# Optimization experiments

Hardware: AMD Instinct MI355X
Metric: run time of the kernel (lower is better)

The kernel has to match this reference:

```python
import jax, jax.numpy as jnp
import numpy as np

HEADS, DIM, SEQ_LEN, MEM_LEN, CMEM_LEN, CMEM_RATIO = 16, 1024, 512, 512, 128, 4
DIM_H = DIM // HEADS


def shift(x):
    # relative-position shift trick, same as torch version
    *lead, i, j = x.shape
    x = jnp.concatenate([x, jnp.zeros((*lead, i, i), x.dtype)], -1)
    l = i + j - 1
    x = x.reshape(*lead, -1)
    pad = (-x.shape[-1]) % l
    x = jnp.concatenate([x, jnp.zeros((*lead, pad), x.dtype)], -1)
    x = x.reshape(*lead, -1, l)
    return x[..., :i, i - 1:]


def merge_heads(t):
    b, n, _ = t.shape
    return t.reshape(b, n, HEADS, DIM_H).transpose(0, 2, 1, 3)  # [b,h,n,dh]


def conv_compress(mem, conv_w, conv_b):
    # Conv1d(dim, dim, k=ratio, stride=ratio) == blockwise einsum
    b, L, e = mem.shape
    blocks = mem.reshape(b, L // CMEM_RATIO, CMEM_RATIO, e)
    return jnp.einsum('bmri,oir->bmo', blocks, conv_w) + conv_b


def full_attn(q, k, v):
    dots = jnp.einsum('bhid,bhjd->bhij', q, k) * (q.shape[-1] ** -0.5)
    attn = jax.nn.softmax(dots, axis=-1)
    return jnp.einsum('bhij,bhjd->bhid', attn, v)


def setup_inputs() -> dict:
    key = jax.random.key(0)
    ks = jax.random.split(key, 10)
    b = 8
    kv_len = CMEM_LEN + MEM_LEN + SEQ_LEN
    s = 0.02
    return {
        'x': jax.random.normal(ks[0], (b, SEQ_LEN, DIM), jnp.float32),
        'mem': jax.random.normal(ks[1], (b, MEM_LEN, DIM), jnp.float32),
        'cmem': jax.random.normal(ks[2], (b, CMEM_LEN, DIM), jnp.float32),
        'pos_emb': jax.random.normal(ks[3], (HEADS, kv_len, DIM_H), jnp.float32),
        'Wq': jax.random.normal(ks[4], (DIM, DIM), jnp.float32) * s,
        'Wkv': jax.random.normal(ks[5], (DIM, 2 * DIM), jnp.float32) * s,
        'Wout': jax.random.normal(ks[6], (DIM, DIM), jnp.float32) * s,
        'bout': jnp.zeros((DIM,), jnp.float32),
        'conv_w': jax.random.normal(ks[7], (DIM, DIM, CMEM_RATIO), jnp.float32) * s,
        'conv_b': jnp.zeros((DIM,), jnp.float32),
    }


def reference(x, mem, cmem, pos_emb, Wq, Wkv, Wout, bout, conv_w, conv_b):
    b, t, e = x.shape
    scale = DIM_H ** -0.5
    mem_len, cmem_len = mem.shape[1], cmem.shape[1]

    q = x @ Wq
    kv_input = jnp.concatenate([cmem, mem, x], axis=1)
    kv_len = kv_input.shape[1]
    k, v = jnp.split(kv_input @ Wkv, 2, axis=-1)
    q, k, v = map(merge_heads, (q, k, v))  # [b,h,n,dh]

    dots = jnp.einsum('bhid,bhjd->bhij', q, k) * scale
    pe = pos_emb[:, -kv_len:].astype(q.dtype)
    pos_dots = shift(jnp.einsum('bhid,hjd->bhij', q, pe) * scale)
    dots = dots + pos_dots

    attn = jax.nn.softmax(dots, axis=-1)
    weights = attn
    out = jnp.einsum('bhij,bhjd->bhid', attn, v)
    out = out.transpose(0, 2, 1, 3).reshape(b, t, -1)
    logits = out @ Wout + bout

    # memory update (queue_fifo with length mem_len)
    queue = jnp.concatenate([mem, x], axis=1)
    old_mem, new_mem = queue[:, :-MEM_LEN], queue[:, -MEM_LEN:]
    # old_mem length (512) divisible by cmem_ratio -> no padding branch
    compressed_mem = conv_compress(old_mem, conv_w, conv_b)
    new_cmem = jnp.concatenate([cmem, compressed_mem], axis=1)[:, -CMEM_LEN:]

    # auxiliary reconstruction loss (detached paths)
    old_mem_d = jax.lax.stop_gradient(old_mem)
    cm2 = conv_compress(old_mem_d, conv_w, conv_b)
    cmem_k, cmem_v = jnp.split(cm2 @ jax.lax.stop_gradient(Wkv), 2, axis=-1)
    cmem_k, cmem_v = map(merge_heads, (cmem_k, cmem_v))
    lo = kv_len - min(mem_len, MEM_LEN) - SEQ_LEN
    hi = kv_len - SEQ_LEN
    old_mem_k = jax.lax.stop_gradient(k[:, :, lo:hi])
    old_mem_v = jax.lax.stop_gradient(v[:, :, lo:hi])
    q_d = jax.lax.stop_gradient(q)
    aux_loss = jnp.mean((full_attn(q_d, old_mem_k, old_mem_v)
                         - full_attn(q_d, cmem_k, cmem_v)) ** 2)

    return logits, new_mem, new_cmem, aux_loss, weights
```

## Files before the change

### kernel.cpp

```cpp
#include <hip/hip_runtime.h>
#include <cstdint>


typedef __bf16 bf16;
typedef __bf16 bf16x2 __attribute__((ext_vector_type(2)));
typedef __bf16 bf16x4 __attribute__((ext_vector_type(4)));
typedef __bf16 bf16x8 __attribute__((ext_vector_type(8)));
typedef float  f32x2  __attribute__((ext_vector_type(2)));
typedef float  f32x4  __attribute__((ext_vector_type(4)));

#define GLOAD_LDS16(g, l) \
    __builtin_amdgcn_global_load_lds((const __attribute__((address_space(1))) void*)(g), \
                                     (__attribute__((address_space(3))) void*)(l), 16, 0, 0)

template<int AMODE, int EPI>
__device__ __forceinline__ void gemm_body(
    int bx, int by, int bz,
    const bf16* __restrict__ A, const bf16* __restrict__ B2,
    float* __restrict__ C, bf16* __restrict__ outB, bf16* __restrict__ vT,
    int N, int K, int lda, int ldbt, int ldc,
    const float* __restrict__ bias, int vrows,
    const bf16* __restrict__ gcmem, const bf16* __restrict__ gmem,
    const bf16* __restrict__ gx,
    bf16* As, bf16* Bs)
{
    int row0 = by * 128, col0 = bx * 128;
    int tid = threadIdx.x;
    int kofs = (EPI == 8) ? bz * K : 0;

    int lane = tid & 63, wid = tid >> 6;
    int wr = wid >> 1, wc = wid & 1;
    int fr = lane & 15, fq = lane >> 4;

    int srow = lane >> 2;
    int sc16 = (lane & 3) ^ ((lane >> 3) & 3);
    const bf16* aq[2];
    const bf16* bq[2];
    bf16* as_dst[2];
    bf16* bs_dst[2];
#pragma unroll
    for (int t = 0; t < 2; t++) {
        int gr = row0 + wid * 32 + t * 16 + srow;
        const bf16* ap;
        if (AMODE == 0) {
            ap = A + (long)gr * lda + kofs;
        } else {
            int bb = gr / 1152, rr = gr - bb * 1152;
            ap = (rr < 128) ? (gcmem + ((long)bb * 128 + rr) * 1024)
               : (rr < 640) ? (gmem + ((long)bb * 512 + (rr - 128)) * 1024)
                            : (gx   + ((long)bb * 512 + (rr - 640)) * 1024);
        }
        aq[t] = ap + sc16 * 8;
        int gc = col0 + wid * 32 + t * 16 + srow;
        bq[t] = B2 + (long)gc * ldbt + kofs + sc16 * 8;
        as_dst[t] = &As[(wid * 32 + t * 16) * 32];
        bs_dst[t] = &Bs[(wid * 32 + t * 16) * 32];
    }

    int sfq = (fq ^ ((fr >> 1) & 3)) * 8;

    f32x4 acc[4][4];
#pragma unroll
    for (int i = 0; i < 4; i++)
#pragma unroll
        for (int j = 0; j < 4; j++) acc[i][j] = (f32x4){0.f, 0.f, 0.f, 0.f};

    for (int k0 = 0; k0 < K; k0 += 32) {
#pragma unroll
        for (int t = 0; t < 2; t++) {
            GLOAD_LDS16(aq[t] + k0, as_dst[t]);
            GLOAD_LDS16(bq[t] + k0, bs_dst[t]);
        }
        __syncthreads();

        bf16x8 af[4], bfv[4];
#pragma unroll
        for (int i = 0; i < 4; i++)
            af[i] = *(const bf16x8*)&As[(wr * 64 + i * 16 + fr) * 32 + sfq];
#pragma unroll
        for (int j = 0; j < 4; j++)
            bfv[j] = *(const bf16x8*)&Bs[(wc * 64 + j * 16 + fr) * 32 + sfq];
#pragma unroll
        for (int i = 0; i < 4; i++)
#pragma unroll
            for (int j = 0; j < 4; j++)
                acc[i][j] = __builtin_amdgcn_mfma_f32_16x16x32_bf16(af[i], bfv[j], acc[i][j], 0, 0, 0);
        __syncthreads();
    }

#pragma unroll
    for (int i = 0; i < 4; i++) {
#pragma unroll
        for (int j = 0; j < 4; j++) {
#pragma unroll
            for (int g = 0; g < 4; g++) {
                int r = row0 + wr * 64 + i * 16 + fq * 4 + g;
                int c = col0 + wc * 64 + j * 16 + fr;
                float v = acc[i][j][g];
                if (EPI == 0) {
                    if (bias) v += bias[c];
                    C[(long)r * ldc + c] = v;
                } else if (EPI == 6) {
                    if (bias) v += bias[c];
                    __builtin_nontemporal_store(v, &C[(long)r * ldc + c]);
                } else if (EPI == 8) {
                    C[((long)bz << 20) + (long)r * 1024 + c] = v;
                } else if (EPI == 4) {
                    outB[(long)r * ldc + c] = (bf16)v;
                } else {
                    if (c < 1024) {
                        outB[(long)r * 1024 + c] = (bf16)v;
                    } else {
                        int d = c - 1024; int hh = d >> 6; d &= 63;
                        int bb = r / vrows; int j2 = r - bb * vrows;
                        vT[(((long)(bb * 16 + hh)) * 64 + d) * vrows + j2] = (bf16)v;
                    }
                }
            }
        }
    }
}

__device__ __forceinline__ void aux_body(
    int bx, int by,
    const bf16* __restrict__ qb, const bf16* __restrict__ kb,
    const bf16* __restrict__ ckb,
    const bf16* __restrict__ vTb, const bf16* __restrict__ cvT,
    float* __restrict__ partials,
    bf16* qs, bf16* upool, bf16* vt, float* wred)
{
    int z = by;
    int b = z >> 4, h = z & 15;
    int r0 = bx * 128;
    int tid = threadIdx.x;
    int lane = tid & 63, wid = tid >> 6;
    int fr = lane & 15, fq = lane >> 4;

#pragma unroll
    for (int t = 0; t < 4; t++) {
        int e = tid + 256 * t; int rr = e >> 3, c8 = (e & 7) * 8;
        *(bf16x8*)&qs[rr * 72 + c8] = *(const bf16x8*)&qb[((long)(b * 512 + r0 + rr)) * 1024 + h * 64 + c8];
    }

    float o1[2][4][4];
    f32x4 oaccv[2][4];
    float mrow[2][4], lrow[2][4];
    f32x4 sacc[2][8];
    float local = 0.f;

    for (int pass = 0; pass < 2; pass++) {
#pragma unroll
        for (int i = 0; i < 2; i++)
#pragma unroll
            for (int g = 0; g < 4; g++) { mrow[i][g] = -3.4e38f; lrow[i][g] = 0.f; }
#pragma unroll
        for (int i = 0; i < 2; i++)
#pragma unroll
            for (int jd = 0; jd < 4; jd++) oaccv[i][jd] = (f32x4){0.f, 0.f, 0.f, 0.f};

        int nchunk = pass ? 1 : 4;
        for (int jt = 0; jt < nchunk; jt++) {
            __syncthreads();
            if (pass == 0) {
                long base = (long)(b * 1152 + 128 + jt * 128);
#pragma unroll
                for (int t = 0; t < 4; t++) {
                    int e = tid + 256 * t; int j = e >> 3, c8 = (e & 7) * 8;
                    *(bf16x8*)&upool[j * 72 + c8] = *(const bf16x8*)&kb[(base + j) * 1024 + h * 64 + c8];
                }
#pragma unroll
                for (int t = 0; t < 4; t++) {
                    int e = tid + 256 * t; int d = e >> 4, j8 = (e & 15) * 8;
                    *(bf16x8*)&vt[d * 136 + j8] =
                        *(const bf16x8*)&vTb[((long)z * 64 + d) * 1152 + 128 + jt * 128 + j8];
                }
            } else {
#pragma unroll
                for (int t = 0; t < 4; t++) {
                    int e = tid + 256 * t; int j = e >> 3, c8 = (e & 7) * 8;
                    *(bf16x8*)&upool[j * 72 + c8] = *(const bf16x8*)&ckb[((long)(b * 128 + j)) * 1024 + h * 64 + c8];
                }
#pragma unroll
                for (int t = 0; t < 4; t++) {
                    int e = tid + 256 * t; int d = e >> 4, j8 = (e & 15) * 8;
                    *(bf16x8*)&vt[d * 136 + j8] = *(const bf16x8*)&cvT[((long)z * 64 + d) * 128 + j8];
                }
            }
            __syncthreads();

#pragma unroll
            for (int i = 0; i < 2; i++)
#pragma unroll
                for (int j = 0; j < 8; j++) sacc[i][j] = (f32x4){0.f, 0.f, 0.f, 0.f};
#pragma unroll
            for (int s = 0; s < 2; s++) {
                bf16x8 af[2], bfv[8];
#pragma unroll
                for (int i = 0; i < 2; i++)
                    af[i] = *(const bf16x8*)&qs[(wid * 32 + i * 16 + fr) * 72 + s * 32 + fq * 8];
#pragma unroll
                for (int j = 0; j < 8; j++)
                    bfv[j] = *(const bf16x8*)&upool[(j * 16 + fr) * 72 + s * 32 + fq * 8];
#pragma unroll
                for (int i = 0; i < 2; i++)
#pragma unroll
                    for (int j = 0; j < 8; j++)
                        sacc[i][j] = __builtin_amdgcn_mfma_f32_16x16x32_bf16(af[i], bfv[j], sacc[i][j], 0, 0, 0);
            }
            __syncthreads();

#pragma unroll
            for (int i = 0; i < 2; i++) {
#pragma unroll
                for (int g = 0; g < 4; g++) {
                    float mx = -3.4e38f;
#pragma unroll
                    for (int j = 0; j < 8; j++) mx = fmaxf(mx, sacc[i][j][g]);
                    mx *= 0.125f;
#pragma unroll
                    for (int msk = 1; msk <= 8; msk <<= 1) mx = fmaxf(mx, __shfl_xor(mx, msk, 64));
                    float mnew = fmaxf(mrow[i][g], mx);
                    float alpha = __expf(mrow[i][g] - mnew);
                    mrow[i][g] = mnew;
                    float sum = 0.f;
                    int prow = (wid * 32 + i * 16 + fq * 4 + g) * 136;
#pragma unroll
                    for (int j = 0; j < 8; j++) {
                        float p = __expf(sacc[i][j][g] * 0.125f - mnew);
                        sum += p;
                        upool[prow + j * 16 + fr] = (bf16)p;
                    }
#pragma unroll
                    for (int msk = 1; msk <= 8; msk <<= 1) sum += __shfl_xor(sum, msk, 16);
                    lrow[i][g] = lrow[i][g] * alpha + sum;
#pragma unroll
                    for (int jd = 0; jd < 4; jd++) oaccv[i][jd][g] *= alpha;
                }
            }
            __syncthreads();

#pragma unroll
            for (int s2 = 0; s2 < 4; s2++) {
                bf16x8 pa[2], vb[4];
#pragma unroll
                for (int i = 0; i < 2; i++)
                    pa[i] = *(const bf16x8*)&upool[(wid * 32 + i * 16 + fr) * 136 + s2 * 32 + fq * 8];
#pragma unroll
                for (int jd = 0; jd < 4; jd++)
                    vb[jd] = *(const bf16x8*)&vt[(jd * 16 + fr) * 136 + s2 * 32 + fq * 8];
#pragma unroll
                for (int i = 0; i < 2; i++)
#pragma unroll
                    for (int jd = 0; jd < 4; jd++)
                        oaccv[i][jd] = __builtin_amdgcn_mfma_f32_16x16x32_bf16(pa[i], vb[jd], oaccv[i][jd], 0, 0, 0);
            }
        }

        if (pass == 0) {
#pragma unroll
            for (int i = 0; i < 2; i++)
#pragma unroll
                for (int jd = 0; jd < 4; jd++)
#pragma unroll
                    for (int g = 0; g < 4; g++)
                        o1[i][jd][g] = oaccv[i][jd][g] / lrow[i][g];
        } else {
#pragma unroll
            for (int i = 0; i < 2; i++)
#pragma unroll
                for (int jd = 0; jd < 4; jd++)
#pragma unroll
                    for (int g = 0; g < 4; g++) {
                        float dd = o1[i][jd][g] - oaccv[i][jd][g] / lrow[i][g];
                        local += dd * dd;
                    }
        }
    }

#pragma unroll
    for (int off = 32; off; off >>= 1) local += __shfl_xor(local, off, 64);
    if (lane == 0) wred[wid] = local;
    __syncthreads();
    if (tid == 0)
        partials[(long)by * 4 + bx] = wred[0] + wred[1] + wred[2] + wred[3];
}

__global__ __launch_bounds__(256)
void gemmA_kernel(const bf16* __restrict__ xb, const bf16* __restrict__ memb,
                  const bf16* __restrict__ cmemb,
                  const bf16* __restrict__ WqTb, const bf16* __restrict__ WkvTb,
                  const bf16* __restrict__ convwTb,
                  bf16* __restrict__ qb, bf16* __restrict__ kb, bf16* __restrict__ vTb,
                  float* __restrict__ pbuf)
{
    __shared__ bf16 As[128 * 32];
    __shared__ bf16 Bs[128 * 32];
    int gid = blockIdx.x;
    if (gid < 1152) {
        gemm_body<1, 5>(gid % 16, gid / 16, 0, nullptr, WkvTb, nullptr, kb, vTb,
                        2048, 1024, 1024, 1024, 2048, nullptr, 1152,
                        cmemb, memb, xb, As, Bs);
    } else if (gid < 1408) {
        int g = gid - 1152;
        gemm_body<0, 4>(g % 8, g / 8, 0, xb, WqTb, nullptr, qb, nullptr,
                        1024, 1024, 1024, 1024, 1024, nullptr, 0,
                        nullptr, nullptr, nullptr, As, Bs);
    } else {
        int g = gid - 1408;
        gemm_body<0, 8>(g % 8, (g / 8) % 8, g / 64, memb, convwTb, pbuf, nullptr, nullptr,
                        1024, 1024, 4096, 4096, 1024, nullptr, 0,
                        nullptr, nullptr, nullptr, As, Bs);
    }
}

__global__ __launch_bounds__(256)
void ckv_kernel(const bf16* __restrict__ ncmemb, const bf16* __restrict__ WkvTb,
                bf16* __restrict__ ckb, bf16* __restrict__ cvT)
{
    __shared__ bf16 As[128 * 32];
    __shared__ bf16 Bs[128 * 32];
    gemm_body<0, 5>(blockIdx.x % 16, blockIdx.x / 16, 0, ncmemb, WkvTb, nullptr, ckb, cvT,
                    2048, 1024, 1024, 1024, 2048, nullptr, 128,
                    nullptr, nullptr, nullptr, As, Bs);
}

#define SSTR 1164

__global__ __launch_bounds__(256)
void attn_fused16(const bf16* __restrict__ qb, const bf16* __restrict__ kb,
                  const bf16* __restrict__ peb, const bf16* __restrict__ vTb,
                  float* __restrict__ weights, bf16* __restrict__ oatb)
{
    int bid = blockIdx.x;
    int w = (bid & 7) * 512 + (bid >> 3);
    int z = w >> 5;
    int b = z >> 4, h = z & 15;
    int r0 = (w & 31) * 16;
    int tid = threadIdx.x;
    int lane = tid & 63, wid = tid >> 6;
    int fr = lane & 15, fq = lane >> 4;

    __shared__ bf16 S[16 * SSTR];

    bf16x8 afr[2];
#pragma unroll
    for (int ks = 0; ks < 2; ks++)
        afr[ks] = *(const bf16x8*)&qb[((long)(b * 512 + r0 + fr)) * 1024 + h * 64 + ks * 32 + fq * 8];

#pragma unroll 3
    for (int ch = 0; ch < 9; ch++) {
        int c0 = ch * 128;
        int jb0 = c0 + 496 - r0 + 32 * wid;

        f32x4 p[3];
#pragma unroll
        for (int ct = 0; ct < 3; ct++) {
            f32x4 a = (f32x4){0.f, 0.f, 0.f, 0.f};
            int j = jb0 + ct * 16 + fr;
            bool ok = (j < 1152);
#pragma unroll
            for (int ks = 0; ks < 2; ks++) {
                bf16x8 bv = {};
                if (ok) bv = *(const bf16x8*)&peb[((long)(h * 1152 + j)) * 64 + ks * 32 + fq * 8];
                a = __builtin_amdgcn_mfma_f32_16x16x32_bf16(afr[ks], bv, a, 0, 0, 0);
            }
            p[ct] = a;
        }

#pragma unroll
        for (int tt = 0; tt < 2; tt++) {
            int cc = 32 * wid + 16 * tt + fr;
            f32x4 a = (f32x4){0.f, 0.f, 0.f, 0.f};
            long krow = (long)(b * 1152 + c0 + cc);
#pragma unroll
            for (int ks = 0; ks < 2; ks++) {
                bf16x8 bv = *(const bf16x8*)&kb[krow * 1024 + h * 64 + ks * 32 + fq * 8];
                a = __builtin_amdgcn_mfma_f32_16x16x32_bf16(afr[ks], bv, a, 0, 0, 0);
            }
#pragma unroll
            for (int g = 0; g < 4; g++) {
                int rr = fq * 4 + g;
                int uu = fr + 15 - rr;
                int src = (uu & 15) | (fq << 4);
                float s0 = __shfl(p[tt][g], src, 64);
                float s1 = __shfl(p[tt + 1][g], src, 64);
                float pv = (uu < 16) ? s0 : s1;
                S[rr * SSTR + c0 + cc] = (bf16)(0.125f * (a[g] + pv));
            }
        }
    }
    __syncthreads();

    for (int rw = 0; rw < 4; rw++) {
        int row = wid * 4 + rw;
        bf16* Srow = &S[row * SSTR];
        bf16x8 v0 = *(const bf16x8*)&Srow[lane * 8];
        bf16x8 v1 = *(const bf16x8*)&Srow[512 + lane * 8];
        bf16x2 v2 = *(const bf16x2*)&Srow[1024 + lane * 2];
        float e[18];
#pragma unroll
        for (int j = 0; j < 8; j++) { e[j] = (float)v0[j]; e[8 + j] = (float)v1[j]; }
        e[16] = (float)v2[0]; e[17] = (float)v2[1];

        float m = e[0];
#pragma unroll
        for (int k = 1; k < 18; k++) m = fmaxf(m, e[k]);
#pragma unroll
        for (int off = 32; off; off >>= 1) m = fmaxf(m, __shfl_xor(m, off, 64));
        float sm = 0.f;
#pragma unroll
        for (int k = 0; k < 18; k++) { e[k] = __expf(e[k] - m); sm += e[k]; }
#pragma unroll
        for (int off = 32; off; off >>= 1) sm += __shfl_xor(sm, off, 64);
        float inv = 1.f / sm;

        bf16x8 w0, w1; bf16x2 w2;
#pragma unroll
        for (int j = 0; j < 8; j++) { w0[j] = (bf16)(e[j] * inv); w1[j] = (bf16)(e[8 + j] * inv); }
        w2[0] = (bf16)(e[16] * inv); w2[1] = (bf16)(e[17] * inv);
        *(bf16x8*)&Srow[lane * 8] = w0;
        *(bf16x8*)&Srow[512 + lane * 8] = w1;
        *(bf16x2*)&Srow[1024 + lane * 2] = w2;
    }
    __syncthreads();

    f32x4 oacc = (f32x4){0.f, 0.f, 0.f, 0.f};
    int dt = wid;
    for (int ch = 0; ch < 9; ch++) {
        int c0 = ch * 128;
#pragma unroll
        for (int ks = 0; ks < 4; ks++) {
            bf16x8 pa = *(const bf16x8*)&S[fr * SSTR + c0 + ks * 32 + fq * 8];
            bf16x8 vb = *(const bf16x8*)&vTb[((long)z * 64 + dt * 16 + fr) * 1152 + c0 + ks * 32 + fq * 8];
            oacc = __builtin_amdgcn_mfma_f32_16x16x32_bf16(pa, vb, oacc, 0, 0, 0);
        }
    }
#pragma unroll
    for (int g = 0; g < 4; g++)
        oatb[((long)(b * 512 + r0 + fq * 4 + g)) * 1024 + h * 64 + dt * 16 + fr] = (bf16)oacc[g];

    for (int rw = 0; rw < 4; rw++) {
        int row = wid * 4 + rw;
        const bf16* Srow = &S[row * SSTR];
        long wbase = ((long)z * 512 + r0 + row) * 1152;
        bf16x8 v0 = *(const bf16x8*)&Srow[lane * 8];
        bf16x8 v1 = *(const bf16x8*)&Srow[512 + lane * 8];
        bf16x2 v2 = *(const bf16x2*)&Srow[1024 + lane * 2];
        f32x4 a0 = { (float)v0[0], (float)v0[1], (float)v0[2], (float)v0[3] };
        f32x4 a1 = { (float)v0[4], (float)v0[5], (float)v0[6], (float)v0[7] };
        f32x4 b0 = { (float)v1[0], (float)v1[1], (float)v1[2], (float)v1[3] };
        f32x4 b1 = { (float)v1[4], (float)v1[5], (float)v1[6], (float)v1[7] };
        f32x2 c0 = { (float)v2[0], (float)v2[1] };
        __builtin_nontemporal_store(a0, (f32x4*)&weights[wbase + lane * 8]);
        __builtin_nontemporal_store(a1, (f32x4*)&weights[wbase + lane * 8 + 4]);
        __builtin_nontemporal_store(b0, (f32x4*)&weights[wbase + 512 + lane * 8]);
        __builtin_nontemporal_store(b1, (f32x4*)&weights[wbase + 512 + lane * 8 + 4]);
        __builtin_nontemporal_store(c0, (f32x2*)&weights[wbase + 1024 + lane * 2]);
    }
}

__global__ __launch_bounds__(256)
void logits_aux_kernel(const bf16* __restrict__ qb, const bf16* __restrict__ kb,
                       const bf16* __restrict__ ckb,
                       const bf16* __restrict__ vTb, const bf16* __restrict__ cvT,
                       float* __restrict__ partials,
                       const bf16* __restrict__ oatb, const bf16* __restrict__ WoutTb,
                       float* __restrict__ out_logits, const float* __restrict__ bout)
{
    __shared__ bf16 pool[35328];
    __shared__ float wred[4];
    int gid = blockIdx.x;
    if (gid < 512) {
        aux_body(gid % 4, gid / 4, qb, kb, ckb, vTb, cvT, partials,
                 pool, pool + 9216, pool + 26624, wred);
    } else {
        int g = gid - 512;
        gemm_body<0, 6>(g % 8, g / 8, 0, oatb, WoutTb, out_logits, nullptr, nullptr,
                        1024, 1024, 1024, 1024, 1024, bout, 0,
                        nullptr, nullptr, nullptr, pool, pool + 4096);
    }
}

__global__ __launch_bounds__(256)
void splitk_reduce(const float* __restrict__ pbuf, const float* __restrict__ bias,
                   float* __restrict__ outF, bf16* __restrict__ outB)
{
    int i = blockIdx.x * 256 + threadIdx.x;
    f32x4 s = reinterpret_cast<const f32x4*>(pbuf)[i];
#pragma unroll
    for (int k = 1; k < 4; k++) {
        f32x4 t = reinterpret_cast<const f32x4*>(pbuf + (long)k * 1048576)[i];
        s[0] += t[0]; s[1] += t[1]; s[2] += t[2]; s[3] += t[3];
    }
    int col4 = (i << 2) & 1023;
    f32x4 bv = *(const f32x4*)&bias[col4];
    s[0] += bv[0]; s[1] += bv[1]; s[2] += bv[2]; s[3] += bv[3];
    reinterpret_cast<f32x4*>(outF)[i] = s;
    bf16x4 h = { (bf16)s[0], (bf16)s[1], (bf16)s[2], (bf16)s[3] };
    reinterpret_cast<bf16x4*>(outB)[i] = h;
}

__device__ __forceinline__ void transpose_body(
    int bx, int by, const float* __restrict__ in, bf16* __restrict__ out,
    int R, int C, float* t )
{
    int c0 = bx * 32, r0 = by * 32;
    int tx = threadIdx.x & 31, ty = threadIdx.x >> 5;
#pragma unroll
    for (int i = 0; i < 32; i += 8)
        t[(ty + i) * 33 + tx] = in[(long)(r0 + ty + i) * C + c0 + tx];
    __syncthreads();
#pragma unroll
    for (int i = 0; i < 32; i += 8)
        out[(long)(c0 + ty + i) * R + r0 + tx] = (bf16)t[tx * 33 + ty + i];
}

__device__ __forceinline__ void convw_body(
    int o, const float* __restrict__ cw, bf16* __restrict__ out, float* t )
{
    const float* src = cw + (long)o * 4096;
    bf16* dst = out + (long)o * 4096;
#pragma unroll
    for (int k = 0; k < 4; k++)
        *(f32x4*)&t[(threadIdx.x + k * 256) * 4] = *(const f32x4*)&src[(threadIdx.x + k * 256) * 4];
    __syncthreads();
#pragma unroll
    for (int k = 0; k < 8; k++) {
        int d2 = 2 * (threadIdx.x + k * 256);
        int pi = ((d2 & 1023) << 2) | (d2 >> 10);
        bf16x2 h = { (bf16)t[pi], (bf16)t[pi + 4] };
        *(bf16x2*)&dst[d2] = h;
    }
}

__global__ __launch_bounds__(256)
void prologue_kernel(const float* __restrict__ Wq, bf16* __restrict__ WqTb,
                     const float* __restrict__ Wkv, bf16* __restrict__ WkvTb,
                     const float* __restrict__ Wout, bf16* __restrict__ WoutTb,
                     const float* __restrict__ conv_w, bf16* __restrict__ convwTb,
                     const float* __restrict__ pe, bf16* __restrict__ peb,
                     const float* __restrict__ x, bf16* __restrict__ xb,
                     const float* __restrict__ mem, bf16* __restrict__ memb,
                     const float* __restrict__ cmem, bf16* __restrict__ cmemb,
                     float* __restrict__ xmirror)
{
    __shared__ float t[4096];
    int gid = blockIdx.x;
    if (gid < 1024) {
        transpose_body(gid & 31, gid >> 5, Wq, WqTb, 1024, 1024, t);
    } else if (gid < 3072) {
        int g = gid - 1024;
        transpose_body(g & 63, g >> 6, Wkv, WkvTb, 1024, 2048, t);
    } else if (gid < 4096) {
        int g = gid - 3072;
        transpose_body(g & 31, g >> 5, Wout, WoutTb, 1024, 1024, t);
    } else if (gid < 5120) {
        convw_body(gid - 4096, conv_w, convwTb, t);
    } else {
        int i0 = (gid - 5120) * 256 + threadIdx.x;
        const int n0 = 294912, n1 = 1048576, n2 = 1048576, n3 = 262144;
        for (int i = i0; i < n0 + n1 + n2 + n3; i += 2048 * 256) {
            const float* src; bf16* dst; int k = i; int seg;
            if (k < n0) { src = pe; dst = peb; seg = 0; }
            else if ((k -= n0) < n1) { src = x; dst = xb; seg = 1; }
            else if ((k -= n1) < n2) { src = mem; dst = memb; seg = 2; }
            else { k -= n2; src = cmem; dst = cmemb; seg = 3; }
            f32x4 f = reinterpret_cast<const f32x4*>(src)[k];
            bf16x4 h = { (bf16)f[0], (bf16)f[1], (bf16)f[2], (bf16)f[3] };
            reinterpret_cast<bf16x4*>(dst)[k] = h;
            if (seg == 1)
                __builtin_nontemporal_store(f, &reinterpret_cast<f32x4*>(xmirror)[k]);
        }
    }
}

__global__ __launch_bounds__(256)
void aux_reduce_kernel(const float* __restrict__ partials, float* __restrict__ out)
{
    int tid = threadIdx.x;
    __shared__ float wred[4];
    float s = 0.f;
    for (int i = tid; i < 512; i += 256) s += partials[i];
#pragma unroll
    for (int off = 32; off; off >>= 1) s += __shfl_xor(s, off, 64);
    if ((tid & 63) == 0) wred[tid >> 6] = s;
    __syncthreads();
    if (tid == 0) out[0] = (wred[0] + wred[1] + wred[2] + wred[3]) * (1.0f / 4194304.0f);
}

extern "C" void kernel_launch(void* const* d_in, const int* in_sizes, int n_in,
                              void* d_out, int out_size, void* d_ws, size_t ws_size,
                              hipStream_t stream)
{
    const float* x      = (const float*)d_in[0];
    const float* mem    = (const float*)d_in[1];
    const float* cmem   = (const float*)d_in[2];
    const float* pe     = (const float*)d_in[3];
    const float* Wq     = (const float*)d_in[4];
    const float* Wkv    = (const float*)d_in[5];
    const float* Wout   = (const float*)d_in[6];
    const float* bout   = (const float*)d_in[7];
    const float* conv_w = (const float*)d_in[8];
    const float* conv_b = (const float*)d_in[9];

    float* out_logits  = (float*)d_out;
    float* out_newmem  = out_logits + 4194304;
    float* out_newcmem = out_newmem + 4194304;
    float* out_aux     = out_newcmem + 1048576;
    float* out_weights = out_aux + 1;

    float* ws       = (float*)d_ws;
    float* partials = ws;
    float* pbuf     = partials + 4096;
    bf16* bws     = (bf16*)(pbuf + 4194304);
    bf16* WqTb    = bws;
    bf16* WkvTb   = WqTb + 1048576;
    bf16* WoutTb  = WkvTb + 2097152;
    bf16* convwTb = WoutTb + 1048576;
    bf16* vTb     = convwTb + 4194304;
    bf16* cvT     = vTb + 9437184;
    bf16* qb      = cvT + 1048576;
    bf16* kb      = qb + 4194304;
    bf16* ckb     = kb + 9437184;
    bf16* peb     = ckb + 1048576;
    bf16* xb      = peb + 1179648;
    bf16* memb    = xb + 4194304;
    bf16* cmemb   = memb + 4194304;
    bf16* ncmemb  = cmemb + 1048576;
    bf16* oatb    = ncmemb + 1048576;

    dim3 blk(256);

    prologue_kernel<<<dim3(7168), blk, 0, stream>>>(
        Wq, WqTb, Wkv, WkvTb, Wout, WoutTb, conv_w, convwTb,
        pe, peb, x, xb, mem, memb, cmem, cmemb, out_newmem);

    gemmA_kernel<<<dim3(1664), blk, 0, stream>>>(
        xb, memb, cmemb, WqTb, WkvTb, convwTb, qb, kb, vTb, pbuf);

    splitk_reduce<<<dim3(1024), blk, 0, stream>>>(pbuf, conv_b, out_newcmem, ncmemb);

    ckv_kernel<<<dim3(128), blk, 0, stream>>>(ncmemb, WkvTb, ckb, cvT);

    attn_fused16<<<dim3(4096), blk, 0, stream>>>(qb, kb, peb, vTb, out_weights, oatb);

    logits_aux_kernel<<<dim3(768), blk, 0, stream>>>(
        qb, kb, ckb, vTb, cvT, partials, oatb, WoutTb, out_logits, bout);

    aux_reduce_kernel<<<dim3(1), blk, 0, stream>>>(partials, out_aux);
}
```

Baseline: 487.7 us.

## Load aux attention Q/K/V fragments directly from global, drop LDS staging and barriers

```diff
diff --git a/kernel.cpp b/kernel.cpp
--- a/kernel.cpp
+++ b/kernel.cpp
@@ -127,7 +127,7 @@
     const bf16* __restrict__ ckb,
     const bf16* __restrict__ vTb, const bf16* __restrict__ cvT,
     float* __restrict__ partials,
-    bf16* qs, bf16* upool, bf16* vt, float* wred)
+    bf16* P, float* wred)
 {
     int z = by;
     int b = z >> 4, h = z & 15;
@@ -136,11 +136,13 @@
     int lane = tid & 63, wid = tid >> 6;
     int fr = lane & 15, fq = lane >> 4;
 
-#pragma unroll
-    for (int t = 0; t < 4; t++) {
-        int e = tid + 256 * t; int rr = e >> 3, c8 = (e & 7) * 8;
-        *(bf16x8*)&qs[rr * 72 + c8] = *(const bf16x8*)&qb[((long)(b * 512 + r0 + rr)) * 1024 + h * 64 + c8];
-    }
+    bf16x8 qf[2][2];
+#pragma unroll
+    for (int i = 0; i < 2; i++)
+#pragma unroll
+        for (int s = 0; s < 2; s++)
+            qf[i][s] = *(const bf16x8*)&qb[((long)(b * 512 + r0 + wid * 32 + i * 16 + fr)) * 1024
+                                           + h * 64 + s * 32 + fq * 8];
 
     float o1[2][4][4];
     f32x4 oaccv[2][4];
@@ -160,54 +162,27 @@
 
         int nchunk = pass ? 1 : 4;
         for (int jt = 0; jt < nchunk; jt++) {
-            __syncthreads();
-            if (pass == 0) {
-                long base = (long)(b * 1152 + 128 + jt * 128);
-#pragma unroll
-                for (int t = 0; t < 4; t++) {
-                    int e = tid + 256 * t; int j = e >> 3, c8 = (e & 7) * 8;
-                    *(bf16x8*)&upool[j * 72 + c8] = *(const bf16x8*)&kb[(base + j) * 1024 + h * 64 + c8];
+#pragma unroll
+            for (int i = 0; i < 2; i++)
+#pragma unroll
+                for (int j = 0; j < 8; j++) sacc[i][j] = (f32x4){0.f, 0.f, 0.f, 0.f};
+#pragma unroll
+            for (int s = 0; s < 2; s++) {
+                bf16x8 bfv[8];
+#pragma unroll
+                for (int j = 0; j < 8; j++) {
+                    long krow = (pass == 0)
+                        ? (long)(b * 1152 + 128 + jt * 128 + j * 16 + fr)
+                        : (long)(b * 128 + j * 16 + fr);
+                    const bf16* src = (pass == 0) ? kb : ckb;
+                    bfv[j] = *(const bf16x8*)&src[krow * 1024 + h * 64 + s * 32 + fq * 8];
                 }
 #pragma unroll
-                for (int t = 0; t < 4; t++) {
-                    int e = tid + 256 * t; int d = e >> 4, j8 = (e & 15) * 8;
-                    *(bf16x8*)&vt[d * 136 + j8] =
-                        *(const bf16x8*)&vTb[((long)z * 64 + d) * 1152 + 128 + jt * 128 + j8];
-                }
-            } else {
-#pragma unroll
-                for (int t = 0; t < 4; t++) {
-                    int e = tid + 256 * t; int j = e >> 3, c8 = (e & 7) * 8;
-                    *(bf16x8*)&upool[j * 72 + c8] = *(const bf16x8*)&ckb[((long)(b * 128 + j)) * 1024 + h * 64 + c8];
-                }
-#pragma unroll
-                for (int t = 0; t < 4; t++) {
-                    int e = tid + 256 * t; int d = e >> 4, j8 = (e & 15) * 8;
-                    *(bf16x8*)&vt[d * 136 + j8] = *(const bf16x8*)&cvT[((long)z * 64 + d) * 128 + j8];
-                }
+                for (int i = 0; i < 2; i++)
+#pragma unroll
+                    for (int j = 0; j < 8; j++)
+                        sacc[i][j] = __builtin_amdgcn_mfma_f32_16x16x32_bf16(qf[i][s], bfv[j], sacc[i][j], 0, 0, 0);
             }
-            __syncthreads();
-
-#pragma unroll
-            for (int i = 0; i < 2; i++)
-#pragma unroll
-                for (int j = 0; j < 8; j++) sacc[i][j] = (f32x4){0.f, 0.f, 0.f, 0.f};
-#pragma unroll
-            for (int s = 0; s < 2; s++) {
-                bf16x8 af[2], bfv[8];
-#pragma unroll
-                for (int i = 0; i < 2; i++)
-                    af[i] = *(const bf16x8*)&qs[(wid * 32 + i * 16 + fr) * 72 + s * 32 + fq * 8];
-#pragma unroll
-                for (int j = 0; j < 8; j++)
-                    bfv[j] = *(const bf16x8*)&upool[(j * 16 + fr) * 72 + s * 32 + fq * 8];
-#pragma unroll
-                for (int i = 0; i < 2; i++)
-#pragma unroll
-                    for (int j = 0; j < 8; j++)
-                        sacc[i][j] = __builtin_amdgcn_mfma_f32_16x16x32_bf16(af[i], bfv[j], sacc[i][j], 0, 0, 0);
-            }
-            __syncthreads();
 
 #pragma unroll
             for (int i = 0; i < 2; i++) {
@@ -228,7 +203,7 @@
                     for (int j = 0; j < 8; j++) {
                         float p = __expf(sacc[i][j][g] * 0.125f - mnew);
                         sum += p;
-                        upool[prow + j * 16 + fr] = (bf16)p;
+                        P[prow + j * 16 + fr] = (bf16)p;
                     }
 #pragma unroll
                     for (int msk = 1; msk <= 8; msk <<= 1) sum += __shfl_xor(sum, msk, 16);
@@ -237,17 +212,22 @@
                     for (int jd = 0; jd < 4; jd++) oaccv[i][jd][g] *= alpha;
                 }
             }
-            __syncthreads();
 
 #pragma unroll
             for (int s2 = 0; s2 < 4; s2++) {
                 bf16x8 pa[2], vb[4];
 #pragma unroll
                 for (int i = 0; i < 2; i++)
-                    pa[i] = *(const bf16x8*)&upool[(wid * 32 + i * 16 + fr) * 136 + s2 * 32 + fq * 8];
-#pragma unroll
-                for (int jd = 0; jd < 4; jd++)
-                    vb[jd] = *(const bf16x8*)&vt[(jd * 16 + fr) * 136 + s2 * 32 + fq * 8];
+                    pa[i] = *(const bf16x8*)&P[(wid * 32 + i * 16 + fr) * 136 + s2 * 32 + fq * 8];
+#pragma unroll
+                for (int jd = 0; jd < 4; jd++) {
+                    if (pass == 0)
+                        vb[jd] = *(const bf16x8*)&vTb[((long)z * 64 + jd * 16 + fr) * 1152
+                                                      + 128 + jt * 128 + s2 * 32 + fq * 8];
+                    else
+                        vb[jd] = *(const bf16x8*)&cvT[((long)z * 64 + jd * 16 + fr) * 128
+                                                      + s2 * 32 + fq * 8];
+                }
 #pragma unroll
                 for (int i = 0; i < 2; i++)
 #pragma unroll
@@ -467,12 +447,11 @@
                        const bf16* __restrict__ oatb, const bf16* __restrict__ WoutTb,
                        float* __restrict__ out_logits, const float* __restrict__ bout)
 {
-    __shared__ bf16 pool[35328];
+    __shared__ bf16 pool[17408];
     __shared__ float wred[4];
     int gid = blockIdx.x;
     if (gid < 512) {
-        aux_body(gid % 4, gid / 4, qb, kb, ckb, vTb, cvT, partials,
-                 pool, pool + 9216, pool + 26624, wred);
+        aux_body(gid % 4, gid / 4, qb, kb, ckb, vTb, cvT, partials, pool, wred);
     } else {
         int g = gid - 512;
         gemm_body<0, 6>(g % 8, g / 8, 0, oatb, WoutTb, out_logits, nullptr, nullptr,
```

Measured after the change: 508.4 us. 1.04x slower.
